# Kernel optimization log

Hardware: AMD Instinct MI355X
Metric: run time of the kernel (lower is better)

The kernel has to match this reference:

```python
import jax, jax.numpy as jnp
import numpy as np

H = 12
PD = 4
DECAY = 0.99
OFFSETS = (1, 2, 4, 8)
_PI = np.array([0, 0, 0, 1, 1, 2])  # Plucker pair indices i for G(2,4)
_PJ = np.array([1, 2, 3, 2, 3, 3])  # Plucker pair indices j
_J6 = jnp.array([[0, 0, 0, 0, 0, 1], [0, 0, 0, 0, -1, 0], [0, 0, 0, 1, 0, 0],
                 [0, 0, 1, 0, 0, 0], [0, -1, 0, 0, 0, 0], [1, 0, 0, 0, 0, 0]],
                dtype=jnp.float32)


def exterior(p1, p2):
    # p1, p2: [..., 4] -> normalized Plucker coords [..., 6]
    L = p1[..., _PI] * p2[..., _PJ] - p1[..., _PJ] * p2[..., _PI]
    n = jnp.maximum(jnp.linalg.norm(L, axis=-1, keepdims=True), 1e-12)
    return L / n


def setup_inputs() -> dict:
    key = jax.random.key(0)
    ks = jax.random.split(key, 12)
    B, T, D = 2, 2048, 768
    s = 0.02
    return {
        "x": jax.random.normal(ks[0], (B, T, D), jnp.float32),
        "qkv_w": jax.random.normal(ks[1], (3 * D, D), jnp.float32) * s,
        "qkv_b": jnp.zeros((3 * D,), jnp.float32),
        "w1_write": jax.random.normal(ks[2], (PD * H, D), jnp.float32) * s,
        "w2_write": jax.random.normal(ks[3], (PD * H, D), jnp.float32) * s,
        "w1_read": jax.random.normal(ks[4], (PD * H, D), jnp.float32) * s,
        "w2_read": jax.random.normal(ks[5], (PD * H, D), jnp.float32) * s,
        "memv_w": jax.random.normal(ks[6], (D, D), jnp.float32) * s,
        "memv_b": jnp.zeros((D,), jnp.float32),
        "memg_w": jax.random.normal(ks[7], (H, D), jnp.float32) * s,
        "memg_b": jnp.zeros((H,), jnp.float32),
        "mem_scale": jnp.full((H,), 0.1, jnp.float32),
        "out_w": jax.random.normal(ks[8], (D, D), jnp.float32) * s,
        "out_b": jnp.zeros((D,), jnp.float32),
    }


def reference(x, qkv_w, qkv_b, w1_write, w2_write, w1_read, w2_read,
              memv_w, memv_b, memg_w, memg_b, mem_scale, out_w, out_b):
    B, T, D = x.shape
    dh = D // H
    scale = dh ** -0.5

    # --- standard causal attention (dropout disabled / eval mode) ---
    qkv = (x @ qkv_w.T + qkv_b).reshape(B, T, 3, H, dh)
    qkv = jnp.transpose(qkv, (2, 0, 3, 1, 4))  # [3,B,H,T,dh]
    q, k, v = qkv[0], qkv[1], qkv[2]
    att = jnp.einsum('bhtd,bhsd->bhts', q, k) * scale
    upper = jnp.triu(jnp.ones((T, T), bool), 1)
    att = jnp.where(upper, -jnp.inf, att)
    attn = jax.nn.softmax(att, axis=-1)
    seq_out = jnp.einsum('bhts,bhsd->bhtd', attn, v)
    seq_out = jnp.transpose(seq_out, (0, 2, 1, 3)).reshape(B, T, D)

    # --- multi-scale Plucker incidence memory ---
    r1 = (x @ w1_read.T).reshape(B, T, H, PD)
    r2 = (x @ w2_read.T).reshape(B, T, H, PD)
    read_h = jnp.transpose(exterior(r1, r2), (0, 2, 1, 3))  # [B,H,T,6]

    keep = jnp.tril(jnp.ones((T, T), bool), -1)  # strict lower triangle
    total = jnp.zeros((B, H, T, T), x.dtype)
    n_active = 0
    for off in OFFSETS:
        if off >= T:
            continue
        n_active += 1
        x_past = jnp.concatenate(
            [jnp.zeros((B, off, D), x.dtype), x[:, :-off]], axis=1)
        w1 = (x_past @ w1_write.T).reshape(B, T, H, PD)
        w2 = (x @ w2_write.T).reshape(B, T, H, PD)
        wl = exterior(w1, w2)                       # [B,T,H,6]
        jw = jnp.einsum('bthi,ij->bthj', wl, _J6)   # apply J
        jw = jnp.transpose(jw, (0, 2, 1, 3))        # [B,H,T,6]
        inc = jnp.einsum('bhtp,bhsp->bhts', read_h, jw)
        total = total + jnp.where(keep, inc * inc, 0.0)
    total = total / n_active

    pos = jnp.arange(T, dtype=x.dtype)
    decay_w = jnp.where(keep, DECAY ** (pos[:, None] - pos[None, :]), 0.0)
    total = total * decay_w
    mem_score = total.sum(axis=-1)  # [B,H,T]

    mem_val = x @ memv_w.T + memv_b
    gate = jax.nn.sigmoid(x @ memg_w.T + memg_b)  # [B,T,H]
    gated = jax.nn.sigmoid(jnp.transpose(mem_score, (0, 2, 1)) * mem_scale) * gate
    gated = gated.mean(axis=-1, keepdims=True)  # [B,T,1]

    return (seq_out + gated * mem_val) @ out_w.T + out_b
```

## Files before the change

### kernel.cpp

```cpp
#include <hip/hip_runtime.h>

#define H 12
#define T 2048
#define D 768
#define NBT 4096
#define SCALE 0.125f
#define DECAY_F 0.99f
#define NCHK 72
#define NBLK_ATTN (24 * NCHK)
#define NBLK_MS1 192

typedef __attribute__((ext_vector_type(8))) short bf16x8;
typedef __attribute__((ext_vector_type(4))) float f32x4;
typedef __attribute__((ext_vector_type(16))) float f32x16;

static __device__ __forceinline__ ushort f2bf(float f) {
  union { float f; unsigned u; } v; v.f = f;
  unsigned r = (v.u + 0x7FFFu + ((v.u >> 16) & 1u)) >> 16;
  return (ushort)r;
}
static __device__ __forceinline__ float bf2f(ushort u) {
  union { unsigned u; float f; } v; v.u = ((unsigned)u) << 16;
  return v.f;
}
static __device__ __forceinline__ unsigned cvtpk(float lo, float hi) {
  unsigned r;
  asm("v_cvt_pk_bf16_f32 %0, %1, %2" : "=v"(r) : "v"(lo), "v"(hi));
  return r;
}
static __device__ __forceinline__ void swap32(unsigned &a, unsigned &b) {
  asm("v_permlane32_swap_b32 %0, %1" : "+v"(a), "+v"(b));
}

static __device__ __forceinline__ void gload16(const void* g, void* s) {
  __builtin_amdgcn_global_load_lds(
      (const __attribute__((address_space(1))) unsigned int*)g,
      (__attribute__((address_space(3))) unsigned int*)s, 16, 0, 0);
}

__global__ __launch_bounds__(256) void cast_all(
    const float* __restrict__ x, const float* __restrict__ qkv_w,
    const float* __restrict__ memv_w, const float* __restrict__ out_w,
    const float* __restrict__ w1w, const float* __restrict__ w2w,
    const float* __restrict__ w1r, const float* __restrict__ w2r,
    const float* __restrict__ memg_w, ushort* __restrict__ dst)
{
  const size_t i8 = ((size_t)blockIdx.x * 256 + threadIdx.x) * 8;
  const float* src; size_t off;
  if      (i8 < 3145728) { src = x;      off = i8; }
  else if (i8 < 4915200) { src = qkv_w;  off = i8 - 3145728; }
  else if (i8 < 5505024) { src = memv_w; off = i8 - 4915200; }
  else if (i8 < 5541888) { src = w1w;    off = i8 - 5505024; }
  else if (i8 < 5578752) { src = w2w;    off = i8 - 5541888; }
  else if (i8 < 5615616) { src = w1r;    off = i8 - 5578752; }
  else if (i8 < 5652480) { src = w2r;    off = i8 - 5615616; }
  else if (i8 < 5661696) { src = memg_w; off = i8 - 5652480; }
  else if (i8 < 5701632) { *(uint4*)(dst + i8) = make_uint4(0, 0, 0, 0); return; }
  else                   { src = out_w;  off = i8 - 5701632; }
  const float4 a = *(const float4*)(src + off);
  const float4 b = *(const float4*)(src + off + 4);
  bf16x8 o;
  o[0] = (short)f2bf(a.x); o[1] = (short)f2bf(a.y);
  o[2] = (short)f2bf(a.z); o[3] = (short)f2bf(a.w);
  o[4] = (short)f2bf(b.x); o[5] = (short)f2bf(b.y);
  o[6] = (short)f2bf(b.z); o[7] = (short)f2bf(b.w);
  *(bf16x8*)(dst + i8) = o;
}

__global__ __launch_bounds__(512, 2) void gemm8_mega(
    const ushort* __restrict__ A, const ushort* __restrict__ W,
    const float* __restrict__ qkv_b, const float* __restrict__ memv_b,
    ushort* __restrict__ memvp, float* __restrict__ pw,
    float* __restrict__ pmemg,
    ushort* __restrict__ Qb, ushort* __restrict__ Kb, ushort* __restrict__ Vtb)
{
  __shared__ ushort lds[65536];
  const int tid = threadIdx.x;
  const int w = tid >> 6, l = tid & 63;
  const int wm = w >> 2, wn = w & 3;
  const int l15 = l & 15, l4 = l >> 4;

  int bid = blockIdx.x;
  bid = (bid & 7) * 26 + (bid >> 3);
  const int bx = bid % 13, by = bid / 13;
  const int bm = by * 256, bn = bx * 256;

  f32x4 acc[8][4];
#pragma unroll
  for (int i = 0; i < 8; i++)
#pragma unroll
    for (int j = 0; j < 4; j++) acc[i][j] = (f32x4){0.f, 0.f, 0.f, 0.f};

  auto stage = [&](int s, int isB, int h, int kt) {
    const ushort* src = (isB ? W + (size_t)bn * 768 : A + (size_t)bm * 768);
#pragma unroll
    for (int j = 0; j < 2; j++) {
      const int chunk = j * 512 + tid;
      const int r = chunk >> 3, c = chunk & 7;
      const int csrc = c ^ (r & 7);
      gload16(src + (size_t)(h * 128 + r) * 768 + kt * 64 + csrc * 8,
              (char*)lds + s * 65536 + isB * 32768 + h * 16384
                         + (size_t)(j * 512 + w * 64) * 16);
    }
  };
  auto rdA = [&](int s, int mi, int ks) -> bf16x8 {
    const int row = wm * 128 + mi * 16 + l15;
    const int ch = (ks * 4 + l4) ^ (l15 & 7);
    return *(const bf16x8*)((const char*)lds + s * 65536 + row * 128 + ch * 16);
  };
  auto rdB = [&](int s, int ni, int ks) -> bf16x8 {
    const int row = wn * 64 + ni * 16 + l15;
    const int ch = (ks * 4 + l4) ^ (l15 & 7);
    return *(const bf16x8*)((const char*)lds + s * 65536 + 32768 + row * 128 + ch * 16);
  };

  stage(0, 1, 0, 0); stage(0, 1, 1, 0); stage(0, 0, 0, 0); stage(0, 0, 1, 0);

#define MFMA_QUAD(mb, ks)                                                      \
  {                                                                            \
    __builtin_amdgcn_s_setprio(1);                                             \
    _Pragma("unroll")                                                          \
    for (int mi = 0; mi < 4; mi++) {                                           \
      const bf16x8 av = rdA(s, (mb) + mi, (ks));                               \
      acc[(mb)+mi][0] = __builtin_amdgcn_mfma_f32_16x16x32_bf16(av, bq0, acc[(mb)+mi][0], 0, 0, 0); \
      acc[(mb)+mi][1] = __builtin_amdgcn_mfma_f32_16x16x32_bf16(av, bq1, acc[(mb)+mi][1], 0, 0, 0); \
      acc[(mb)+mi][2] = __builtin_amdgcn_mfma_f32_16x16x32_bf16(av, bq2, acc[(mb)+mi][2], 0, 0, 0); \
      acc[(mb)+mi][3] = __builtin_amdgcn_mfma_f32_16x16x32_bf16(av, bq3, acc[(mb)+mi][3], 0, 0, 0); \
    }                                                                          \
    __builtin_amdgcn_s_setprio(0);                                             \
  }

  for (int t = 0; t < 12; t++) {
    const int s = t & 1, sn = s ^ 1;
    const int ktn = (t + 1) % 12;
    bf16x8 bq0, bq1, bq2, bq3;
    stage(sn, 1, 0, ktn);
    asm volatile("s_waitcnt vmcnt(2)" ::: "memory");
    __builtin_amdgcn_s_barrier();
    __builtin_amdgcn_sched_barrier(0);
    bq0 = rdB(s, 0, 0); bq1 = rdB(s, 1, 0); bq2 = rdB(s, 2, 0); bq3 = rdB(s, 3, 0);
    MFMA_QUAD(0, 0);
    __builtin_amdgcn_s_barrier();
    stage(sn, 1, 1, ktn);
    MFMA_QUAD(4, 0);
    __builtin_amdgcn_s_barrier();
    stage(sn, 0, 0, ktn);
    bq0 = rdB(s, 0, 1); bq1 = rdB(s, 1, 1); bq2 = rdB(s, 2, 1); bq3 = rdB(s, 3, 1);
    MFMA_QUAD(0, 1);
    __builtin_amdgcn_s_barrier();
    stage(sn, 0, 1, ktn);
    MFMA_QUAD(4, 1);
    __builtin_amdgcn_s_barrier();
  }

#pragma unroll
  for (int mi = 0; mi < 8; mi++) {
    const int row0 = bm + wm * 128 + mi * 16 + l4 * 4;
    const int b = row0 >> 11, tl = row0 & (T - 1);
#pragma unroll
    for (int ni = 0; ni < 4; ni++) {
      const int col = bn + wn * 64 + ni * 16 + l15;
      const f32x4 a4 = acc[mi][ni];
      if (col < 2304) {
        const float bv = qkv_b[col];
        const int sec = col / 768, cm = col % 768;
        const int h = cm >> 6, d = cm & 63;
        if (sec < 2) {
          ushort* dst = sec ? Kb : Qb;
#pragma unroll
          for (int r = 0; r < 4; r++)
            dst[((size_t)(b * H + h) * T + tl + r) * 64 + d] = f2bf(a4[r] + bv);
        } else {
          uint2 u;
          u.x = (unsigned)f2bf(a4[0] + bv) | ((unsigned)f2bf(a4[1] + bv) << 16);
          u.y = (unsigned)f2bf(a4[2] + bv) | ((unsigned)f2bf(a4[3] + bv) << 16);
          *(uint2*)(Vtb + ((size_t)(b * H + h) * 64 + d) * T + tl) = u;
        }
      } else if (col < 3072) {
        const int c2 = col - 2304;
        const float bv = memv_b[c2];
#pragma unroll
        for (int r = 0; r < 4; r++)
          memvp[(size_t)(row0 + r) * 768 + c2] = f2bf(a4[r] + bv);
      } else if (col < 3276) {
        const int c2 = col - 3072;
        if (c2 < 192) {
          float* pb = pw + (size_t)(c2 / 48) * (H * NBT * 4);
          const int hh = (c2 % 48) >> 2, comp = c2 & 3;
#pragma unroll
          for (int r = 0; r < 4; r++)
            pb[((size_t)hh * NBT + row0 + r) * 4 + comp] = a4[r];
        } else {
#pragma unroll
          for (int r = 0; r < 4; r++)
            pmemg[(size_t)(c2 - 192) * NBT + row0 + r] = a4[r];
        }
      }
    }
  }
}

__global__ __launch_bounds__(256) void gemm_out64(
    const ushort* __restrict__ A, const ushort* __restrict__ W,
    const float* __restrict__ bias, float* __restrict__ C)
{
  __shared__ ushort A_lds[128 * 64];
  __shared__ ushort B_lds[64 * 64];
  const int tid = threadIdx.x;
  const int w = tid >> 6, l = tid & 63;
  const int wm = w >> 1, wn = w & 1;
  const int bm = blockIdx.y * 128, bn = blockIdx.x * 64;
  const int l15 = l & 15, l4 = l >> 4;

  f32x4 acc[4][2];
#pragma unroll
  for (int i = 0; i < 4; i++)
#pragma unroll
    for (int j = 0; j < 2; j++) acc[i][j] = (f32x4){0.f, 0.f, 0.f, 0.f};

  const int srowA = w * 32 + (l >> 3);
  const int srowB = w * 16 + (l >> 3);
  const int scol = (l & 7) * 8;
  const ushort* Ag = A + (size_t)(bm + srowA) * 768 + scol;
  const ushort* Wg = W + (size_t)(bn + srowB) * 768 + scol;
  ushort* Asl = &A_lds[(w * 32) * 64];
  ushort* Bsl = &B_lds[(w * 16) * 64];

  for (int k0 = 0; k0 < 768; k0 += 64) {
#pragma unroll
    for (int i = 0; i < 4; i++)
      gload16(Ag + k0 + i * 8 * 768, Asl + i * 8 * 64);
#pragma unroll
    for (int i = 0; i < 2; i++)
      gload16(Wg + k0 + i * 8 * 768, Bsl + i * 8 * 64);
    __syncthreads();
#pragma unroll
    for (int ks = 0; ks < 2; ks++) {
      bf16x8 af[4], bfr[2];
#pragma unroll
      for (int i = 0; i < 4; i++)
        af[i] = *(const bf16x8*)&A_lds[(wm * 64 + i * 16 + l15) * 64 + ks * 32 + l4 * 8];
#pragma unroll
      for (int i = 0; i < 2; i++)
        bfr[i] = *(const bf16x8*)&B_lds[(wn * 32 + i * 16 + l15) * 64 + ks * 32 + l4 * 8];
#pragma unroll
      for (int mi = 0; mi < 4; mi++)
#pragma unroll
        for (int ni = 0; ni < 2; ni++)
          acc[mi][ni] = __builtin_amdgcn_mfma_f32_16x16x32_bf16(af[mi], bfr[ni], acc[mi][ni], 0, 0, 0);
    }
    __syncthreads();
  }
#pragma unroll
  for (int mi = 0; mi < 4; mi++) {
    const int row0 = bm + wm * 64 + mi * 16 + l4 * 4;
#pragma unroll
    for (int ni = 0; ni < 2; ni++) {
      const int col = bn + wn * 32 + ni * 16 + l15;
      const float bv = bias[col];
#pragma unroll
      for (int r = 0; r < 4; r++)
        C[(size_t)(row0 + r) * 768 + col] = acc[mi][ni][r] + bv;
    }
  }
}

__device__ __forceinline__ void ext_norm6(const float4 a, const float4 b, float* L)
{
  L[0] = a.x * b.y - a.y * b.x;
  L[1] = a.x * b.z - a.z * b.x;
  L[2] = a.x * b.w - a.w * b.x;
  L[3] = a.y * b.z - a.z * b.y;
  L[4] = a.y * b.w - a.w * b.y;
  L[5] = a.z * b.w - a.w * b.z;
  float n2 = L[0]*L[0] + L[1]*L[1] + L[2]*L[2] + L[3]*L[3] + L[4]*L[4] + L[5]*L[5];
  float n = fmaxf(sqrtf(n2), 1e-12f);
  float inv = 1.f / n;
#pragma unroll
  for (int i = 0; i < 6; i++) L[i] *= inv;
}

static __device__ void memscan1_body(
    int bb, char* smem, const float* __restrict__ pw,
    float* __restrict__ Rp, float* __restrict__ G)
{
  const int bh = bb >> 3, chunk = bb & 7;
  const int b = bh / H, h = bh % H;
  const int tid = threadIdx.x;
  float (*S)[22] = (float(*)[22])smem;
  const int t = chunk * 256 + tid;
  const size_t hb = (size_t)h * NBT + (size_t)b * T;
  const float* pw1w = pw + 0 * (size_t)(H * NBT * 4) + hb * 4;
  const float* pw2w = pw + 1 * (size_t)(H * NBT * 4) + hb * 4;
  const float* pw1r = pw + 2 * (size_t)(H * NBT * 4) + hb * 4;
  const float* pw2r = pw + 3 * (size_t)(H * NBT * 4) + hb * 4;

  float Cm[21];
#pragma unroll
  for (int c = 0; c < 21; c++) Cm[c] = 0.f;
  {
    const float4 w2 = *(const float4*)(pw2w + (size_t)t * 4);
    const int offs[4] = {1, 2, 4, 8};
#pragma unroll
    for (int oi = 0; oi < 4; oi++) {
      const int off = offs[oi];
      if (t >= off) {
        const float4 w1 = *(const float4*)(pw1w + (size_t)(t - off) * 4);
        float L[6];
        ext_norm6(w1, w2, L);
        const float Jv[6] = { L[5], -L[4], L[3], L[2], -L[1], L[0] };
        int c = 0;
#pragma unroll
        for (int p = 0; p < 6; p++)
#pragma unroll
          for (int q = p; q < 6; q++) { Cm[c] += Jv[p] * Jv[q]; c++; }
      }
    }
  }
  float R[6];
  {
    const float4 r1 = *(const float4*)(pw1r + (size_t)t * 4);
    const float4 r2 = *(const float4*)(pw2r + (size_t)t * 4);
    ext_norm6(r1, r2, R);
  }

#pragma unroll
  for (int c = 0; c < 21; c++) S[tid][c] = Cm[c];
  __syncthreads();
  float pd = DECAY_F;
  for (int off = 1; off < 256; off <<= 1) {
    float tmpv[21];
#pragma unroll
    for (int c = 0; c < 21; c++) tmpv[c] = (tid >= off) ? S[tid - off][c] : 0.f;
    __syncthreads();
#pragma unroll
    for (int c = 0; c < 21; c++) S[tid][c] += pd * tmpv[c];
    __syncthreads();
    pd *= pd;
  }
  float P[21];
#pragma unroll
  for (int c = 0; c < 21; c++) P[c] = (tid > 0) ? DECAY_F * S[tid - 1][c] : 0.f;

  float part1 = 0.f;
  {
    int c = 0;
#pragma unroll
    for (int p = 0; p < 6; p++) {
      part1 += P[c] * R[p] * R[p]; c++;
#pragma unroll
      for (int q = p + 1; q < 6; q++) { part1 += 2.f * P[c] * R[p] * R[q]; c++; }
    }
  }
  float* rp = Rp + ((size_t)bh * T + t) * 8;
  *(float4*)rp = make_float4(R[0], R[1], R[2], R[3]);
  *(float4*)(rp + 4) = make_float4(R[4], R[5], part1, 0.f);
  if (tid < 21)
    G[((size_t)bh * 8 + chunk) * 21 + tid] = S[255][tid];
}

__global__ __launch_bounds__(256) void attn_memscan(
    const ushort* __restrict__ Qb, const ushort* __restrict__ Kb,
    const ushort* __restrict__ Vtb, ushort* __restrict__ o_part,
    float* __restrict__ rs_part,
    const float* __restrict__ pw, float* __restrict__ Rp, float* __restrict__ G)
{
  __shared__ __align__(16) char smem[36864];

  if (blockIdx.x < NBLK_MS1) {
    memscan1_body(blockIdx.x, smem, pw, Rp, G);
    return;
  }
  const int abid = blockIdx.x - NBLK_MS1;

  typedef ushort row72[72];
  row72* K_lds = (row72*)smem;
  row72* V_lds = (row72*)(smem + 18432);

  const int bh = abid / NCHK;
  const int ci2 = 71 - (abid % NCHK);
  int ci = ci2;
  int qb = 15;
#pragma unroll
  for (int q = 0; q < 16; q++) {
    const int cnt = (q >> 1) + 1;
    if (ci < cnt) { qb = q; break; }
    ci -= cnt;
  }
  const int slot = bh * NCHK + ci2;
  const int t0 = qb * 128;
  const int it0 = ci * 4;
  const int it1 = min(it0 + 4, 2 * qb + 2);

  const int tid = threadIdx.x;
  const int w = tid >> 6;
  const int l = tid & 63;
  const int l31 = l & 31;
  const int lhi = l >> 5;

  bf16x8 qf[4];
  {
    const ushort* qp = Qb + ((size_t)bh * T + t0 + w * 32 + l31) * 64 + 8 * lhi;
#pragma unroll
    for (int kf = 0; kf < 4; kf++) qf[kf] = *(const bf16x8*)(qp + kf * 16);
  }
  f32x16 o0, o1;
#pragma unroll
  for (int r = 0; r < 16; r++) { o0[r] = 0.f; o1[r] = 0.f; }
  float rs = 0.f;

  const int sr = tid >> 2;
  const int scg = (tid & 3) * 16;
  const ushort* ksrc = Kb + ((size_t)bh * T + sr) * 64 + scg;
  const ushort* vsrc = Vtb + ((size_t)bh * 64 + sr) * T + scg;
  const int qlo = t0 + w * 32;
  const int qg = qlo + l31;

  bf16x8 kA0, kA1, vA0, vA1, kB0, kB1, vB0, vB1;
  {
    const size_t sa = (size_t)it0 * 64, sb = sa + 64;
    kA0 = *(const bf16x8*)(ksrc + sa * 64);
    kA1 = *(const bf16x8*)(ksrc + sa * 64 + 8);
    vA0 = *(const bf16x8*)(vsrc + sa);
    vA1 = *(const bf16x8*)(vsrc + sa + 8);
    kB0 = *(const bf16x8*)(ksrc + sb * 64);
    kB1 = *(const bf16x8*)(ksrc + sb * 64 + 8);
    vB0 = *(const bf16x8*)(vsrc + sb);
    vB1 = *(const bf16x8*)(vsrc + sb + 8);
  }

  auto process = [&](int s0, int ro) {
    f32x16 sA, sB;
#pragma unroll
    for (int r = 0; r < 16; r++) { sA[r] = 0.f; sB[r] = 0.f; }
    __builtin_amdgcn_s_setprio(1);
#pragma unroll
    for (int kf = 0; kf < 4; kf++) {
      const bf16x8 ka  = *(const bf16x8*)&K_lds[ro + l31][kf * 16 + 8 * lhi];
      const bf16x8 kb2 = *(const bf16x8*)&K_lds[ro + 32 + l31][kf * 16 + 8 * lhi];
      sA = __builtin_amdgcn_mfma_f32_32x32x16_bf16(ka, qf[kf], sA, 0, 0, 0);
      sB = __builtin_amdgcn_mfma_f32_32x32x16_bf16(kb2, qf[kf], sB, 0, 0, 0);
    }
    __builtin_amdgcn_s_setprio(0);

    const bool nomask = (s0 + 63 <= qlo);
#pragma unroll
    for (int half = 0; half < 2; half++) {
      float pv[16];
#pragma unroll
      for (int r = 0; r < 16; r++) {
        const int srow = (r & 3) + 8 * (r >> 2) + 4 * lhi;
        const float sv = (half == 0) ? sA[r] : sB[r];
        float p = __expf(sv * SCALE);
        if (!nomask && (s0 + half * 32 + srow > qg)) p = 0.f;
        rs += p;
        pv[r] = p;
      }
#pragma unroll
      for (int sub = 0; sub < 2; sub++) {
        const float* p8 = pv + 8 * sub;
        unsigned X = cvtpk(p8[0], p8[1]);
        unsigned Y = cvtpk(p8[4], p8[5]);
        unsigned Z = cvtpk(p8[2], p8[3]);
        unsigned Wd = cvtpk(p8[6], p8[7]);
        swap32(X, Y);
        swap32(Z, Wd);
        union { unsigned u[4]; bf16x8 v; } fr;
        fr.u[0] = X; fr.u[1] = Z; fr.u[2] = Y; fr.u[3] = Wd;
        const int ksl = half * 2 + sub;
        const bf16x8 va = *(const bf16x8*)&V_lds[ro + l31][ksl * 16 + 8 * lhi];
        const bf16x8 vb = *(const bf16x8*)&V_lds[ro + 32 + l31][ksl * 16 + 8 * lhi];
        __builtin_amdgcn_s_setprio(1);
        o0 = __builtin_amdgcn_mfma_f32_32x32x16_bf16(va, fr.v, o0, 0, 0, 0);
        o1 = __builtin_amdgcn_mfma_f32_32x32x16_bf16(vb, fr.v, o1, 0, 0, 0);
        __builtin_amdgcn_s_setprio(0);
      }
    }
  };

  for (int its = it0; its < it1; its += 2) {
    __syncthreads();
    *(bf16x8*)&K_lds[sr][scg]       = kA0;
    *(bf16x8*)&K_lds[sr][scg + 8]   = kA1;
    *(bf16x8*)&V_lds[sr][scg]       = vA0;
    *(bf16x8*)&V_lds[sr][scg + 8]   = vA1;
    *(bf16x8*)&K_lds[64 + sr][scg]     = kB0;
    *(bf16x8*)&K_lds[64 + sr][scg + 8] = kB1;
    *(bf16x8*)&V_lds[64 + sr][scg]     = vB0;
    *(bf16x8*)&V_lds[64 + sr][scg + 8] = vB1;
    __syncthreads();
    if (its + 2 < it1) {
      const size_t sa = (size_t)(its + 2) * 64, sb = sa + 64;
      kA0 = *(const bf16x8*)(ksrc + sa * 64);
      kA1 = *(const bf16x8*)(ksrc + sa * 64 + 8);
      vA0 = *(const bf16x8*)(vsrc + sa);
      vA1 = *(const bf16x8*)(vsrc + sa + 8);
      kB0 = *(const bf16x8*)(ksrc + sb * 64);
      kB1 = *(const bf16x8*)(ksrc + sb * 64 + 8);
      vB0 = *(const bf16x8*)(vsrc + sb);
      vB1 = *(const bf16x8*)(vsrc + sb + 8);
    }
    const int s0A = its * 64, s0B = s0A + 64;
    if (s0A <= qlo + 31) process(s0A, 0);
    if (s0B <= qlo + 31) process(s0B, 64);
  }

  rs += __shfl_xor(rs, 32);

  const int brow = w * 32 + l31;
  ushort* ob = o_part + ((size_t)slot * 128 + brow) * 64;
  float* rsb = rs_part + (size_t)slot * 128;
#pragma unroll
  for (int r = 0; r < 16; r += 2) {
    const int d = (r & 3) + 8 * (r >> 2) + 4 * lhi;
    *(unsigned*)(ob + d)      = cvtpk(o0[r], o0[r + 1]);
    *(unsigned*)(ob + 32 + d) = cvtpk(o1[r], o1[r + 1]);
  }
  if (l < 32) rsb[brow] = rs;
}

__global__ __launch_bounds__(256) void gatescan(
    const float* __restrict__ G, const float* __restrict__ Rp,
    const float* __restrict__ pmemg, const float* __restrict__ memg_b,
    const float* __restrict__ mem_scale, float* __restrict__ gate12)
{
  __shared__ float E[8][21];
  const int bh = blockIdx.x;
  const int b = bh / H, h = bh % H;
  const int tid = threadIdx.x;
  if (tid < 21) {
    float e = 0.f;
    const float d256 = 0.076314145f;
    for (int c = 0; c < 8; c++) {
      E[c][tid] = e;
      e = DECAY_F * G[((size_t)bh * 8 + c) * 21 + tid] + d256 * e;
    }
  }
  __syncthreads();
  const int chunk = tid >> 5;
  const int base = (tid & 31) * 8;
  float Ec[21];
#pragma unroll
  for (int c = 0; c < 21; c++) Ec[c] = E[chunk][c];

  const float msc = mem_scale[h];
  const float gb = memg_b[h];
  const size_t hb = (size_t)h * NBT + (size_t)b * T;
  const size_t rb = (size_t)b * T;
  float dj = __powf(DECAY_F, (float)base);
  for (int j = 0; j < 8; j++) {
    const int tl = chunk * 256 + base + j;
    const float* rp = Rp + ((size_t)bh * T + tl) * 8;
    const float4 q0 = *(const float4*)rp;
    const float4 q1 = *(const float4*)(rp + 4);
    const float R[6] = { q0.x, q0.y, q0.z, q0.w, q1.x, q1.y };
    const float part1 = q1.z;
    float qd = 0.f;
    {
      int c = 0;
#pragma unroll
      for (int p = 0; p < 6; p++) {
        qd += Ec[c] * R[p] * R[p]; c++;
#pragma unroll
        for (int q = p + 1; q < 6; q++) { qd += 2.f * Ec[c] * R[p] * R[q]; c++; }
      }
    }
    const float score = (part1 + dj * qd) * 0.25f;
    const float g1 = 1.f / (1.f + __expf(-score * msc));
    const float graw = pmemg[hb + tl] + gb;
    const float g2 = 1.f / (1.f + __expf(-graw));
    gate12[(rb + tl) * H + h] = g1 * g2;
    dj *= DECAY_F;
  }
}

__global__ __launch_bounds__(256) void reduce_fuse(
    const ushort* __restrict__ o_part, const float* __restrict__ rs_part,
    const ushort* __restrict__ memv, const float* __restrict__ gate12,
    ushort* __restrict__ zb)
{
  const int idx = blockIdx.x * 256 + threadIdx.x;
  const int row = idx / 96, c = (idx % 96) * 8;
  const int h = c >> 6, d0 = c & 63;
  const int b = row >> 11, tl = row & (T - 1);
  const int qb = tl >> 7, rloc = tl & 127;
  const int m = qb >> 1;
  const int cnt = m + 1;
  const int base = m * (m + 1) + (qb & 1) * (m + 1);
  const size_t bid0 = (size_t)(b * H + h) * NCHK + base;

  float o[8] = {0.f, 0.f, 0.f, 0.f, 0.f, 0.f, 0.f, 0.f};
  float rsum = 0.f;
  for (int ci = 0; ci < cnt; ci++) {
    const bf16x8 pv = *(const bf16x8*)(o_part + ((bid0 + ci) * 128 + rloc) * 64 + d0);
#pragma unroll
    for (int j = 0; j < 8; j++) o[j] += bf2f((ushort)pv[j]);
    rsum += rs_part[(bid0 + ci) * 128 + rloc];
  }
  const float inv = 1.f / rsum;

  const float* gp = gate12 + (size_t)row * H;
  float gs = 0.f;
#pragma unroll
  for (int j = 0; j < 12; j++) gs += gp[j];
  const float g = gs * (1.f / 12.f);

  const bf16x8 mv = *(const bf16x8*)(memv + (size_t)row * D + c);
  bf16x8 z;
#pragma unroll
  for (int j = 0; j < 8; j++)
    z[j] = (short)f2bf(o[j] * inv + g * bf2f((ushort)mv[j]));
  *(bf16x8*)(zb + (size_t)row * D + c) = z;
}

extern "C" void kernel_launch(void* const* d_in, const int* in_sizes, int n_in,
                              void* d_out, int out_size, void* d_ws, size_t ws_size,
                              hipStream_t stream)
{
  const float* x      = (const float*)d_in[0];
  const float* qkv_w  = (const float*)d_in[1];
  const float* qkv_b  = (const float*)d_in[2];
  const float* w1w    = (const float*)d_in[3];
  const float* w2w    = (const float*)d_in[4];
  const float* w1r    = (const float*)d_in[5];
  const float* w2r    = (const float*)d_in[6];
  const float* memv_w = (const float*)d_in[7];
  const float* memv_b = (const float*)d_in[8];
  const float* memg_w = (const float*)d_in[9];
  const float* memg_b = (const float*)d_in[10];
  const float* mem_scale = (const float*)d_in[11];
  const float* out_w  = (const float*)d_in[12];
  const float* out_b  = (const float*)d_in[13];
  float* out = (float*)d_out;

  float* ws    = (float*)d_ws;
  float* pw    = ws;
  float* pmemg = pw + (size_t)4 * H * NBT * 4;
  float* gate12 = pmemg + (size_t)H * NBT;
  float* rs_part = gate12 + (size_t)NBT * H;
  float* Rp    = rs_part + (size_t)NBLK_ATTN * 128;
  float* G     = Rp + (size_t)24 * T * 8;
  ushort* memv = (ushort*)(G + 24 * 8 * 21 + 24);
  ushort* Xb  = memv + (size_t)NBT * D;
  ushort* Wb  = Xb + (size_t)NBT * D;
  ushort* Qb  = Wb + (size_t)NBT * D;
  ushort* Kb  = Qb + (size_t)24 * T * 64;
  ushort* Vtb = Kb + (size_t)24 * T * 64;
  ushort* zb  = Vtb + (size_t)24 * T * 64;
  ushort* o_part = zb + (size_t)NBT * D;

  const ushort* W_out = Wb + (size_t)3328 * 768;

  dim3 blk(256);
  cast_all<<<dim3(3072), blk, 0, stream>>>(x, qkv_w, memv_w, out_w,
                                           w1w, w2w, w1r, w2r, memg_w, Xb);

  gemm8_mega<<<dim3(16 * 13), dim3(512), 0, stream>>>(
      Xb, Wb, qkv_b, memv_b, memv, pw, pmemg, Qb, Kb, Vtb);

  attn_memscan<<<dim3(NBLK_ATTN + NBLK_MS1), blk, 0, stream>>>(
      Qb, Kb, Vtb, o_part, rs_part, pw, Rp, G);

  gatescan<<<dim3(24), blk, 0, stream>>>(G, Rp, pmemg, memg_b, mem_scale, gate12);

  reduce_fuse<<<dim3(NBT * 96 / 256), blk, 0, stream>>>(o_part, rs_part, memv,
                                                        gate12, zb);
  gemm_out64<<<dim3(12, 32), blk, 0, stream>>>(zb, W_out, out_b, out);
}
```

Measured before the change: 123.3 us.

## Drop split-K attention chunks, normalize in-kernel, widen output GEMM tile

Each attention block now handles a whole 128-row query block over the full causal range, so there are 384 blocks instead of 1728 chunked ones. It normalizes by the row sum and writes bf16 output directly, which removes the partial-output and row-sum buffers and the reduction in the fuse kernel. The output GEMM tile grows to 128x128 (192 blocks), exp is switched to exp2 with a folded constant, and the row-sum is split into four accumulators. The trade-off is worse load balance across the causal triangle and fewer blocks to fill the GPU, in exchange for less memory traffic and a simpler reduction.

```diff
diff --git a/kernel.cpp b/kernel.cpp
--- a/kernel.cpp
+++ b/kernel.cpp
@@ -6,9 +6,9 @@
 #define NBT 4096
 #define SCALE 0.125f
 #define DECAY_F 0.99f
-#define NCHK 72
-#define NBLK_ATTN (24 * NCHK)
 #define NBLK_MS1 192
+#define NBLK_ATTN 384
+#define EXP2C 0.18033688011f
 
 typedef __attribute__((ext_vector_type(8))) short bf16x8;
 typedef __attribute__((ext_vector_type(4))) float f32x4;
@@ -200,53 +200,50 @@
   }
 }
 
-__global__ __launch_bounds__(256) void gemm_out64(
+__global__ __launch_bounds__(256) void gemm_mfma128(
     const ushort* __restrict__ A, const ushort* __restrict__ W,
-    const float* __restrict__ bias, float* __restrict__ C)
+    const float* __restrict__ bias, float* __restrict__ C, int ldc)
 {
   __shared__ ushort A_lds[128 * 64];
-  __shared__ ushort B_lds[64 * 64];
+  __shared__ ushort B_lds[128 * 64];
   const int tid = threadIdx.x;
   const int w = tid >> 6, l = tid & 63;
   const int wm = w >> 1, wn = w & 1;
-  const int bm = blockIdx.y * 128, bn = blockIdx.x * 64;
+  const int bm = blockIdx.y * 128, bn = blockIdx.x * 128;
   const int l15 = l & 15, l4 = l >> 4;
 
-  f32x4 acc[4][2];
+  f32x4 acc[4][4];
 #pragma unroll
   for (int i = 0; i < 4; i++)
 #pragma unroll
-    for (int j = 0; j < 2; j++) acc[i][j] = (f32x4){0.f, 0.f, 0.f, 0.f};
-
-  const int srowA = w * 32 + (l >> 3);
-  const int srowB = w * 16 + (l >> 3);
+    for (int j = 0; j < 4; j++) acc[i][j] = (f32x4){0.f, 0.f, 0.f, 0.f};
+
+  const int srow = w * 32 + (l >> 3);
   const int scol = (l & 7) * 8;
-  const ushort* Ag = A + (size_t)(bm + srowA) * 768 + scol;
-  const ushort* Wg = W + (size_t)(bn + srowB) * 768 + scol;
+  const ushort* Ag = A + (size_t)(bm + srow) * 768 + scol;
+  const ushort* Wg = W + (size_t)(bn + srow) * 768 + scol;
   ushort* Asl = &A_lds[(w * 32) * 64];
-  ushort* Bsl = &B_lds[(w * 16) * 64];
+  ushort* Bsl = &B_lds[(w * 32) * 64];
 
   for (int k0 = 0; k0 < 768; k0 += 64) {
 #pragma unroll
-    for (int i = 0; i < 4; i++)
+    for (int i = 0; i < 4; i++) {
       gload16(Ag + k0 + i * 8 * 768, Asl + i * 8 * 64);
-#pragma unroll
-    for (int i = 0; i < 2; i++)
       gload16(Wg + k0 + i * 8 * 768, Bsl + i * 8 * 64);
+    }
     __syncthreads();
 #pragma unroll
     for (int ks = 0; ks < 2; ks++) {
-      bf16x8 af[4], bfr[2];
-#pragma unroll
-      for (int i = 0; i < 4; i++)
-        af[i] = *(const bf16x8*)&A_lds[(wm * 64 + i * 16 + l15) * 64 + ks * 32 + l4 * 8];
-#pragma unroll
-      for (int i = 0; i < 2; i++)
-        bfr[i] = *(const bf16x8*)&B_lds[(wn * 32 + i * 16 + l15) * 64 + ks * 32 + l4 * 8];
+      bf16x8 af[4], bfr[4];
+#pragma unroll
+      for (int i = 0; i < 4; i++) {
+        af[i]  = *(const bf16x8*)&A_lds[(wm * 64 + i * 16 + l15) * 64 + ks * 32 + l4 * 8];
+        bfr[i] = *(const bf16x8*)&B_lds[(wn * 64 + i * 16 + l15) * 64 + ks * 32 + l4 * 8];
+      }
 #pragma unroll
       for (int mi = 0; mi < 4; mi++)
 #pragma unroll
-        for (int ni = 0; ni < 2; ni++)
+        for (int ni = 0; ni < 4; ni++)
           acc[mi][ni] = __builtin_amdgcn_mfma_f32_16x16x32_bf16(af[mi], bfr[ni], acc[mi][ni], 0, 0, 0);
     }
     __syncthreads();
@@ -255,12 +252,12 @@
   for (int mi = 0; mi < 4; mi++) {
     const int row0 = bm + wm * 64 + mi * 16 + l4 * 4;
 #pragma unroll
-    for (int ni = 0; ni < 2; ni++) {
-      const int col = bn + wn * 32 + ni * 16 + l15;
+    for (int ni = 0; ni < 4; ni++) {
+      const int col = bn + wn * 64 + ni * 16 + l15;
       const float bv = bias[col];
 #pragma unroll
       for (int r = 0; r < 4; r++)
-        C[(size_t)(row0 + r) * 768 + col] = acc[mi][ni][r] + bv;
+        C[(size_t)(row0 + r) * ldc + col] = acc[mi][ni][r] + bv;
     }
   }
 }
@@ -361,8 +358,7 @@
 
 __global__ __launch_bounds__(256) void attn_memscan(
     const ushort* __restrict__ Qb, const ushort* __restrict__ Kb,
-    const ushort* __restrict__ Vtb, ushort* __restrict__ o_part,
-    float* __restrict__ rs_part,
+    const ushort* __restrict__ Vtb, ushort* __restrict__ seqb,
     const float* __restrict__ pw, float* __restrict__ Rp, float* __restrict__ G)
 {
   __shared__ __align__(16) char smem[36864];
@@ -377,20 +373,11 @@
   row72* K_lds = (row72*)smem;
   row72* V_lds = (row72*)(smem + 18432);
 
-  const int bh = abid / NCHK;
-  const int ci2 = 71 - (abid % NCHK);
-  int ci = ci2;
-  int qb = 15;
-#pragma unroll
-  for (int q = 0; q < 16; q++) {
-    const int cnt = (q >> 1) + 1;
-    if (ci < cnt) { qb = q; break; }
-    ci -= cnt;
-  }
-  const int slot = bh * NCHK + ci2;
+  const int bh = abid >> 4;
+  const int qb = 15 - (abid & 15);
+  const int b = bh / H, h = bh % H;
   const int t0 = qb * 128;
-  const int it0 = ci * 4;
-  const int it1 = min(it0 + 4, 2 * qb + 2);
+  const int it1 = 2 * qb + 2;
 
   const int tid = threadIdx.x;
   const int w = tid >> 6;
@@ -407,7 +394,7 @@
   f32x16 o0, o1;
 #pragma unroll
   for (int r = 0; r < 16; r++) { o0[r] = 0.f; o1[r] = 0.f; }
-  float rs = 0.f;
+  float rs0 = 0.f, rs1 = 0.f, rs2 = 0.f, rs3 = 0.f;
 
   const int sr = tid >> 2;
   const int scg = (tid & 3) * 16;
@@ -418,15 +405,14 @@
 
   bf16x8 kA0, kA1, vA0, vA1, kB0, kB1, vB0, vB1;
   {
-    const size_t sa = (size_t)it0 * 64, sb = sa + 64;
-    kA0 = *(const bf16x8*)(ksrc + sa * 64);
-    kA1 = *(const bf16x8*)(ksrc + sa * 64 + 8);
-    vA0 = *(const bf16x8*)(vsrc + sa);
-    vA1 = *(const bf16x8*)(vsrc + sa + 8);
-    kB0 = *(const bf16x8*)(ksrc + sb * 64);
-    kB1 = *(const bf16x8*)(ksrc + sb * 64 + 8);
-    vB0 = *(const bf16x8*)(vsrc + sb);
-    vB1 = *(const bf16x8*)(vsrc + sb + 8);
+    kA0 = *(const bf16x8*)(ksrc);
+    kA1 = *(const bf16x8*)(ksrc + 8);
+    vA0 = *(const bf16x8*)(vsrc);
+    vA1 = *(const bf16x8*)(vsrc + 8);
+    kB0 = *(const bf16x8*)(ksrc + (size_t)64 * 64);
+    kB1 = *(const bf16x8*)(ksrc + (size_t)64 * 64 + 8);
+    vB0 = *(const bf16x8*)(vsrc + 64);
+    vB1 = *(const bf16x8*)(vsrc + 64 + 8);
   }
 
   auto process = [&](int s0, int ro) {
@@ -451,11 +437,14 @@
       for (int r = 0; r < 16; r++) {
         const int srow = (r & 3) + 8 * (r >> 2) + 4 * lhi;
         const float sv = (half == 0) ? sA[r] : sB[r];
-        float p = __expf(sv * SCALE);
+        float p = exp2f(sv * EXP2C);
         if (!nomask && (s0 + half * 32 + srow > qg)) p = 0.f;
-        rs += p;
         pv[r] = p;
       }
+      rs0 += pv[0] + pv[1];  rs1 += pv[2] + pv[3];
+      rs2 += pv[4] + pv[5];  rs3 += pv[6] + pv[7];
+      rs0 += pv[8] + pv[9];  rs1 += pv[10] + pv[11];
+      rs2 += pv[12] + pv[13]; rs3 += pv[14] + pv[15];
 #pragma unroll
       for (int sub = 0; sub < 2; sub++) {
         const float* p8 = pv + 8 * sub;
@@ -478,7 +467,7 @@
     }
   };
 
-  for (int its = it0; its < it1; its += 2) {
+  for (int its = 0; its < it1; its += 2) {
     __syncthreads();
     *(bf16x8*)&K_lds[sr][scg]       = kA0;
     *(bf16x8*)&K_lds[sr][scg + 8]   = kA1;
@@ -505,18 +494,18 @@
     if (s0B <= qlo + 31) process(s0B, 64);
   }
 
+  float rs = (rs0 + rs1) + (rs2 + rs3);
   rs += __shfl_xor(rs, 32);
+  const float inv = 1.f / rs;
 
   const int brow = w * 32 + l31;
-  ushort* ob = o_part + ((size_t)slot * 128 + brow) * 64;
-  float* rsb = rs_part + (size_t)slot * 128;
+  ushort* sp = seqb + ((size_t)(b * T + t0 + brow)) * D + h * 64;
 #pragma unroll
   for (int r = 0; r < 16; r += 2) {
     const int d = (r & 3) + 8 * (r >> 2) + 4 * lhi;
-    *(unsigned*)(ob + d)      = cvtpk(o0[r], o0[r + 1]);
-    *(unsigned*)(ob + 32 + d) = cvtpk(o1[r], o1[r + 1]);
-  }
-  if (l < 32) rsb[brow] = rs;
+    *(unsigned*)(sp + d)      = cvtpk(o0[r] * inv, o0[r + 1] * inv);
+    *(unsigned*)(sp + 32 + d) = cvtpk(o1[r] * inv, o1[r + 1] * inv);
+  }
 }
 
 __global__ __launch_bounds__(256) void gatescan(
@@ -574,30 +563,12 @@
   }
 }
 
-__global__ __launch_bounds__(256) void reduce_fuse(
-    const ushort* __restrict__ o_part, const float* __restrict__ rs_part,
-    const ushort* __restrict__ memv, const float* __restrict__ gate12,
-    ushort* __restrict__ zb)
+__global__ __launch_bounds__(256) void fuse_z(
+    const ushort* __restrict__ seqb, const ushort* __restrict__ memv,
+    const float* __restrict__ gate12, ushort* __restrict__ zb)
 {
   const int idx = blockIdx.x * 256 + threadIdx.x;
   const int row = idx / 96, c = (idx % 96) * 8;
-  const int h = c >> 6, d0 = c & 63;
-  const int b = row >> 11, tl = row & (T - 1);
-  const int qb = tl >> 7, rloc = tl & 127;
-  const int m = qb >> 1;
-  const int cnt = m + 1;
-  const int base = m * (m + 1) + (qb & 1) * (m + 1);
-  const size_t bid0 = (size_t)(b * H + h) * NCHK + base;
-
-  float o[8] = {0.f, 0.f, 0.f, 0.f, 0.f, 0.f, 0.f, 0.f};
-  float rsum = 0.f;
-  for (int ci = 0; ci < cnt; ci++) {
-    const bf16x8 pv = *(const bf16x8*)(o_part + ((bid0 + ci) * 128 + rloc) * 64 + d0);
-#pragma unroll
-    for (int j = 0; j < 8; j++) o[j] += bf2f((ushort)pv[j]);
-    rsum += rs_part[(bid0 + ci) * 128 + rloc];
-  }
-  const float inv = 1.f / rsum;
 
   const float* gp = gate12 + (size_t)row * H;
   float gs = 0.f;
@@ -605,11 +576,12 @@
   for (int j = 0; j < 12; j++) gs += gp[j];
   const float g = gs * (1.f / 12.f);
 
+  const bf16x8 sv = *(const bf16x8*)(seqb + (size_t)row * D + c);
   const bf16x8 mv = *(const bf16x8*)(memv + (size_t)row * D + c);
   bf16x8 z;
 #pragma unroll
   for (int j = 0; j < 8; j++)
-    z[j] = (short)f2bf(o[j] * inv + g * bf2f((ushort)mv[j]));
+    z[j] = (short)f2bf(bf2f((ushort)sv[j]) + g * bf2f((ushort)mv[j]));
   *(bf16x8*)(zb + (size_t)row * D + c) = z;
 }
 
@@ -637,8 +609,7 @@
   float* pw    = ws;
   float* pmemg = pw + (size_t)4 * H * NBT * 4;
   float* gate12 = pmemg + (size_t)H * NBT;
-  float* rs_part = gate12 + (size_t)NBT * H;
-  float* Rp    = rs_part + (size_t)NBLK_ATTN * 128;
+  float* Rp    = gate12 + (size_t)NBT * H;
   float* G     = Rp + (size_t)24 * T * 8;
   ushort* memv = (ushort*)(G + 24 * 8 * 21 + 24);
   ushort* Xb  = memv + (size_t)NBT * D;
@@ -646,8 +617,8 @@
   ushort* Qb  = Wb + (size_t)NBT * D;
   ushort* Kb  = Qb + (size_t)24 * T * 64;
   ushort* Vtb = Kb + (size_t)24 * T * 64;
-  ushort* zb  = Vtb + (size_t)24 * T * 64;
-  ushort* o_part = zb + (size_t)NBT * D;
+  ushort* seqb = Vtb + (size_t)24 * T * 64;
+  ushort* zb  = seqb + (size_t)NBT * D;
 
   const ushort* W_out = Wb + (size_t)3328 * 768;
 
@@ -658,12 +629,11 @@
   gemm8_mega<<<dim3(16 * 13), dim3(512), 0, stream>>>(
       Xb, Wb, qkv_b, memv_b, memv, pw, pmemg, Qb, Kb, Vtb);
 
-  attn_memscan<<<dim3(NBLK_ATTN + NBLK_MS1), blk, 0, stream>>>(
-      Qb, Kb, Vtb, o_part, rs_part, pw, Rp, G);
+  attn_memscan<<<dim3(NBLK_MS1 + NBLK_ATTN), blk, 0, stream>>>(
+      Qb, Kb, Vtb, seqb, pw, Rp, G);
 
   gatescan<<<dim3(24), blk, 0, stream>>>(G, Rp, pmemg, memg_b, mem_scale, gate12);
 
-  reduce_fuse<<<dim3(NBT * 96 / 256), blk, 0, stream>>>(o_part, rs_part, memv,
-                                                        gate12, zb);
-  gemm_out64<<<dim3(12, 32), blk, 0, stream>>>(zb, W_out, out_b, out);
-}
+  fuse_z<<<dim3(NBT * 96 / 256), blk, 0, stream>>>(seqb, memv, gate12, zb);
+  gemm_mfma128<<<dim3(6, 32), blk, 0, stream>>>(zb, W_out, out_b, out, 768);
+}
```

After: 161.1 us. 30.6% more time.
